# Performance work log

Hardware: AMD Instinct MI355X
Metric: run time of the kernel (lower is better)

## Reference

```python
import jax, jax.numpy as jnp
import numpy as np

SCALE = 8.0  # cfg.TEST_SCALE (eval path)


def setup_inputs() -> dict:
    key = jax.random.key(0)
    ks = jax.random.split(key, 5)
    N, D, F, NC = 65536, 1024, 300, 81
    return {
        "x": jax.random.normal(ks[0], (N, D), dtype=jnp.float32),
        "W_cls": jax.random.normal(ks[1], (1, D), dtype=jnp.float32) * 0.01,
        "b_cls": jnp.zeros((1,), dtype=jnp.float32),
        "W_sem": jax.random.normal(ks[2], (F, D), dtype=jnp.float32) * 0.01,
        "b_sem": jnp.zeros((F,), dtype=jnp.float32),
        "W_bbox": jax.random.normal(ks[3], (NC * 4, D), dtype=jnp.float32) * 0.001,
        "b_bbox": jnp.zeros((NC * 4,), dtype=jnp.float32),
        "sem_matrix": jax.random.normal(ks[4], (NC - 1, F), dtype=jnp.float32),
    }


def reference(x, W_cls, b_cls, W_sem, b_sem, W_bbox, b_bbox, sem_matrix):
    # b_score: Linear(D, 1)
    b_score = x @ W_cls.T + b_cls                      # [N, 1]
    # sem: Linear(D, F)
    sem = x @ W_sem.T + b_sem                          # [N, F]
    # eval path: scale * L2-row-normalized semantic matrix
    sm = SCALE * sem_matrix / jnp.linalg.norm(sem_matrix, axis=1, keepdims=True)
    # the original per-class repeat/mul/sum loop == one GEMM
    cls_score = sem @ sm.T                             # [N, NC-1]
    scores = jnp.concatenate([b_score, cls_score], axis=1)  # [N, NC]
    bbox_deltas = x @ W_bbox.T + b_bbox                # [N, NC*4]
    return (scores, bbox_deltas)
```

## Files before the change

kernel.cpp:

```cpp
#include <hip/hip_runtime.h>
#include <hip/hip_bf16.h>
#include <stdint.h>

#define KDIM 1024
#define NPAD 512
#define NCOLS 405
#define SCORE_COLS 81
#define BBOX_COLS 324
#define NROWS 65536
#define FDIM 300


typedef short v8s __attribute__((ext_vector_type(8)));
typedef float v4f __attribute__((ext_vector_type(4)));

typedef __attribute__((address_space(3))) uint32_t lds_u32_t;
typedef __attribute__((address_space(1))) uint32_t glb_u32_t;

__device__ __forceinline__ void async16(void* lds, const void* g) {
    __builtin_amdgcn_global_load_lds((const glb_u32_t*)g, (lds_u32_t*)lds, 16, 0, 0);
}

__device__ __forceinline__ uint16_t f2bf(float f) {
    union { float f; uint32_t u; } c; c.f = f;
    uint32_t r = c.u + 0x7FFFu + ((c.u >> 16) & 1u);
    return (uint16_t)(r >> 16);
}

__device__ __forceinline__ size_t wt_off(int row, int k) {
    return (size_t)(k >> 5) * (NPAD * 32) + (size_t)row * 32 + (k & 31);
}

__global__ void fill_w(const float* __restrict__ Wcls, const float* __restrict__ bcls,
                       const float* __restrict__ Wbbox, const float* __restrict__ bbbox,
                       uint16_t* __restrict__ Wt, float* __restrict__ bt) {
    int idx = blockIdx.x * 256 + threadIdx.x;
    int row = idx >> 10, k = idx & 1023;
    if (!(row >= 1 && row < 81)) {
        float v;
        if (row == 0) v = Wcls[k];
        else if (row < 81 + BBOX_COLS) v = Wbbox[(size_t)(row - 81) * KDIM + k];
        else v = 0.f;
        Wt[wt_off(row, k)] = f2bf(v);
    }
    if (k == 0 && !(row >= 1 && row < 81)) {
        float b;
        if (row == 0) b = bcls[0];
        else if (row < 81 + BBOX_COLS) b = bbbox[row - 81];
        else b = 0.f;
        bt[row] = b;
    }
}

__global__ void fill_w_sem(const float* __restrict__ Wsem, const float* __restrict__ bsem,
                           const float* __restrict__ semm,
                           uint16_t* __restrict__ Wt, float* __restrict__ bt) {
    const int n = blockIdx.x;
    const int kq = blockIdx.y;
    const int tid = threadIdx.x;
    __shared__ float s_row[FDIM];
    __shared__ float red[256];
    __shared__ float s_scale, s_bdot;

    const float* sr = semm + (size_t)n * FDIM;
    float p = 0.f, pb = 0.f;
    for (int f = tid; f < FDIM; f += 256) {
        float v = sr[f];
        s_row[f] = v;
        p += v * v;
        pb += v * bsem[f];
    }
    red[tid] = p; __syncthreads();
    for (int s = 128; s > 0; s >>= 1) { if (tid < s) red[tid] += red[tid + s]; __syncthreads(); }
    float norm2 = red[0]; __syncthreads();
    red[tid] = pb; __syncthreads();
    for (int s = 128; s > 0; s >>= 1) { if (tid < s) red[tid] += red[tid + s]; __syncthreads(); }
    if (tid == 0) { s_scale = 8.0f / sqrtf(norm2); s_bdot = red[0]; }
    __syncthreads();
    const float scale = s_scale;
    if (kq == 0 && tid == 0) bt[1 + n] = scale * s_bdot;

    const int k = kq * 256 + tid;
    float acc = 0.f;
    #pragma unroll 8
    for (int f = 0; f < FDIM; ++f) acc += s_row[f] * Wsem[(size_t)f * KDIM + k];
    Wt[wt_off(1 + n, k)] = f2bf(scale * acc);
}

#define A_STRIDE 36
#define A_BUF_ELEMS (64 * A_STRIDE)
#define B_BUF_ELEMS (NPAD * 32)
#define SMEM_BYTES (2 * A_BUF_ELEMS * 2 + 2 * B_BUF_ELEMS * 2)

__device__ __forceinline__ void compute_tile(const uint16_t* As, const uint16_t* Bs,
                                             int wc, int l16, int quad,
                                             v4f acc[4][4]) {
    v8s a[4], b[4];
    #pragma unroll
    for (int mi = 0; mi < 4; ++mi)
        a[mi] = *(const v8s*)&As[(mi * 16 + l16) * A_STRIDE + quad * 8];
    #pragma unroll
    for (int ni = 0; ni < 4; ++ni)
        b[ni] = *(const v8s*)&Bs[(wc * 64 + ni * 16 + l16) * 32 + quad * 8];
    #pragma unroll
    for (int mi = 0; mi < 4; ++mi)
        #pragma unroll
        for (int ni = 0; ni < 4; ++ni)
            acc[mi][ni] = __builtin_amdgcn_mfma_f32_16x16x32_bf16(a[mi], b[ni], acc[mi][ni], 0, 0, 0);
}

__global__ __launch_bounds__(512, 4) void gemm_fused(
        const float* __restrict__ x, const uint16_t* __restrict__ Wt,
        const float* __restrict__ bt, float* __restrict__ out) {
    const int tid = threadIdx.x;
    const int wave = tid >> 6, lane = tid & 63;
    const int wc = wave;
    const int quad = lane >> 4, l16 = lane & 15;
    const int mtile = blockIdx.x;

    __shared__ __align__(16) char smem[SMEM_BYTES];
    uint16_t* As = (uint16_t*)smem;
    uint16_t* Bs = (uint16_t*)(smem + 2 * A_BUF_ELEMS * 2);

    const float* xb = x + (size_t)mtile * 64 * KDIM;

    const int colbase = wc * 64;
    float bias[4];
    #pragma unroll
    for (int ni = 0; ni < 4; ++ni) bias[ni] = bt[colbase + ni * 16 + l16];

    v4f acc[4][4];
    #pragma unroll
    for (int mi = 0; mi < 4; ++mi)
        #pragma unroll
        for (int ni = 0; ni < 4; ++ni)
            acc[mi][ni] = v4f{0.f, 0.f, 0.f, 0.f};

    const int am = tid >> 3, akc = tid & 7;
    float4 av;

    #pragma unroll
    for (int i = 0; i < 4; ++i) {
        int c = i * 512 + tid;
        async16(&Bs[0 * B_BUF_ELEMS + c * 8], Wt + (size_t)c * 8);
    }
    av = *(const float4*)(xb + (size_t)am * KDIM + akc * 4);
    {
        __hip_bfloat162 lo = __float22bfloat162_rn(make_float2(av.x, av.y));
        __hip_bfloat162 hi = __float22bfloat162_rn(make_float2(av.z, av.w));
        uint2 p; p.x = *(uint32_t*)&lo; p.y = *(uint32_t*)&hi;
        *(uint2*)&As[0 * A_BUF_ELEMS + am * A_STRIDE + akc * 4] = p;
    }

    for (int kt = 0; kt < 31; ++kt) {
        const int buf = kt & 1;
        __syncthreads();
        #pragma unroll
        for (int i = 0; i < 4; ++i) {
            int c = i * 512 + tid;
            async16(&Bs[(buf ^ 1) * B_BUF_ELEMS + c * 8],
                    Wt + (size_t)(kt + 1) * B_BUF_ELEMS + (size_t)c * 8);
        }
        av = *(const float4*)(xb + (size_t)am * KDIM + (kt + 1) * 32 + akc * 4);
        compute_tile(&As[buf * A_BUF_ELEMS], &Bs[buf * B_BUF_ELEMS], wc, l16, quad, acc);
        {
            __hip_bfloat162 lo = __float22bfloat162_rn(make_float2(av.x, av.y));
            __hip_bfloat162 hi = __float22bfloat162_rn(make_float2(av.z, av.w));
            uint2 p; p.x = *(uint32_t*)&lo; p.y = *(uint32_t*)&hi;
            *(uint2*)&As[(buf ^ 1) * A_BUF_ELEMS + am * A_STRIDE + akc * 4] = p;
        }
    }
    __syncthreads();
    compute_tile(&As[1 * A_BUF_ELEMS], &Bs[1 * B_BUF_ELEMS], wc, l16, quad, acc);

    const int rowbase = mtile * 64;
    float* eps = (float*)smem;
    float* outb = out + (size_t)NROWS * SCORE_COLS;
    #pragma unroll
    for (int h = 0; h < 2; ++h) {
        __syncthreads();
        #pragma unroll
        for (int mi2 = 0; mi2 < 2; ++mi2) {
            const int mi = h * 2 + mi2;
            #pragma unroll
            for (int ni = 0; ni < 4; ++ni) {
                const int col = colbase + ni * 16 + l16;
                if (col < NCOLS) {
                    #pragma unroll
                    for (int r = 0; r < 4; ++r)
                        eps[(mi2 * 16 + quad * 4 + r) * 409 + col] = acc[mi][ni][r] + bias[ni];
                }
            }
        }
        __syncthreads();
        const int row0 = rowbase + h * 32;
        for (int idx = tid; idx < 32 * SCORE_COLS; idx += 512) {
            int r = idx / SCORE_COLS, c = idx - r * SCORE_COLS;
            out[(size_t)(row0 + r) * SCORE_COLS + c] = eps[r * 409 + c];
        }
        for (int idx = tid; idx < 32 * BBOX_COLS; idx += 512) {
            int r = idx / BBOX_COLS, c = idx - r * BBOX_COLS;
            outb[(size_t)(row0 + r) * BBOX_COLS + c] = eps[r * 409 + SCORE_COLS + c];
        }
    }
}

extern "C" void kernel_launch(void* const* d_in, const int* in_sizes, int n_in,
                              void* d_out, int out_size, void* d_ws, size_t ws_size,
                              hipStream_t stream) {
    const float* x     = (const float*)d_in[0];
    const float* Wcls  = (const float*)d_in[1];
    const float* bcls  = (const float*)d_in[2];
    const float* Wsem  = (const float*)d_in[3];
    const float* bsem  = (const float*)d_in[4];
    const float* Wbbox = (const float*)d_in[5];
    const float* bbbox = (const float*)d_in[6];
    const float* semm  = (const float*)d_in[7];
    float* out = (float*)d_out;

    uint16_t* Wt = (uint16_t*)d_ws;
    float*    bt = (float*)((char*)d_ws + (size_t)NPAD * KDIM * 2);

    fill_w<<<dim3(2048), dim3(256), 0, stream>>>(Wcls, bcls, Wbbox, bbbox, Wt, bt);
    fill_w_sem<<<dim3(80, 4), dim3(256), 0, stream>>>(Wsem, bsem, semm, Wt, bt);
    gemm_fused<<<dim3(1024), dim3(512), 0, stream>>>(x, Wt, bt, out);
}
```

Before: 524.7 us.

## Load weight fragments directly from global into registers, skip B LDS staging

The GEMM stops staging the weight tile in LDS. Each wave now loads its bf16 weight fragments straight from global (L2-resident) into registers and prefetches the next k-slab while the MFMAs run. The padded column count drops from 512 to 416, so the last waves skip the MMA work on padding columns. The A tile uses a triple-buffered LDS ring with a single barrier per k-step, and outputs are written with nontemporal stores. Smaller LDS use may allow more resident blocks, but the wave workload is now uneven and every block reads the weights from L2 itself.

```diff
diff --git a/kernel.cpp b/kernel.cpp
--- a/kernel.cpp
+++ b/kernel.cpp
@@ -3,23 +3,17 @@
 #include <stdint.h>
 
 #define KDIM 1024
-#define NPAD 512
+#define NPAD 416
 #define NCOLS 405
 #define SCORE_COLS 81
 #define BBOX_COLS 324
 #define NROWS 65536
 #define FDIM 300
+#define SLAB (NPAD * 32)
 
 
 typedef short v8s __attribute__((ext_vector_type(8)));
 typedef float v4f __attribute__((ext_vector_type(4)));
-
-typedef __attribute__((address_space(3))) uint32_t lds_u32_t;
-typedef __attribute__((address_space(1))) uint32_t glb_u32_t;
-
-__device__ __forceinline__ void async16(void* lds, const void* g) {
-    __builtin_amdgcn_global_load_lds((const glb_u32_t*)g, (lds_u32_t*)lds, 16, 0, 0);
-}
 
 __device__ __forceinline__ uint16_t f2bf(float f) {
     union { float f; uint32_t u; } c; c.f = f;
@@ -28,7 +22,7 @@
 }
 
 __device__ __forceinline__ size_t wt_off(int row, int k) {
-    return (size_t)(k >> 5) * (NPAD * 32) + (size_t)row * 32 + (k & 31);
+    return (size_t)(k >> 5) * SLAB + (size_t)row * 32 + (k & 31);
 }
 
 __global__ void fill_w(const float* __restrict__ Wcls, const float* __restrict__ bcls,
@@ -89,24 +83,14 @@
 
 #define A_STRIDE 36
 #define A_BUF_ELEMS (64 * A_STRIDE)
-#define B_BUF_ELEMS (NPAD * 32)
-#define SMEM_BYTES (2 * A_BUF_ELEMS * 2 + 2 * B_BUF_ELEMS * 2)
-
-__device__ __forceinline__ void compute_tile(const uint16_t* As, const uint16_t* Bs,
-                                             int wc, int l16, int quad,
-                                             v4f acc[4][4]) {
-    v8s a[4], b[4];
-    #pragma unroll
-    for (int mi = 0; mi < 4; ++mi)
-        a[mi] = *(const v8s*)&As[(mi * 16 + l16) * A_STRIDE + quad * 8];
-    #pragma unroll
-    for (int ni = 0; ni < 4; ++ni)
-        b[ni] = *(const v8s*)&Bs[(wc * 64 + ni * 16 + l16) * 32 + quad * 8];
-    #pragma unroll
-    for (int mi = 0; mi < 4; ++mi)
-        #pragma unroll
-        for (int ni = 0; ni < 4; ++ni)
-            acc[mi][ni] = __builtin_amdgcn_mfma_f32_16x16x32_bf16(a[mi], b[ni], acc[mi][ni], 0, 0, 0);
+#define EPS_STRIDE 409
+#define SMEM_BYTES (32 * EPS_STRIDE * 4)
+
+__device__ __forceinline__ void stcvt(uint16_t* p, float4 av) {
+    __hip_bfloat162 lo = __float22bfloat162_rn(make_float2(av.x, av.y));
+    __hip_bfloat162 hi = __float22bfloat162_rn(make_float2(av.z, av.w));
+    uint2 v; v.x = *(uint32_t*)&lo; v.y = *(uint32_t*)&hi;
+    *(uint2*)p = v;
 }
 
 __global__ __launch_bounds__(512, 4) void gemm_fused(
@@ -114,20 +98,15 @@
         const float* __restrict__ bt, float* __restrict__ out) {
     const int tid = threadIdx.x;
     const int wave = tid >> 6, lane = tid & 63;
-    const int wc = wave;
     const int quad = lane >> 4, l16 = lane & 15;
     const int mtile = blockIdx.x;
+    const int NT = (wave < 6) ? 4 : (wave == 6 ? 2 : 0);
 
     __shared__ __align__(16) char smem[SMEM_BYTES];
     uint16_t* As = (uint16_t*)smem;
-    uint16_t* Bs = (uint16_t*)(smem + 2 * A_BUF_ELEMS * 2);
 
     const float* xb = x + (size_t)mtile * 64 * KDIM;
-
-    const int colbase = wc * 64;
-    float bias[4];
-    #pragma unroll
-    for (int ni = 0; ni < 4; ++ni) bias[ni] = bt[colbase + ni * 16 + l16];
+    const int colbase = wave * 64;
 
     v4f acc[4][4];
     #pragma unroll
@@ -137,45 +116,58 @@
             acc[mi][ni] = v4f{0.f, 0.f, 0.f, 0.f};
 
     const int am = tid >> 3, akc = tid & 7;
-    float4 av;
-
-    #pragma unroll
-    for (int i = 0; i < 4; ++i) {
-        int c = i * 512 + tid;
-        async16(&Bs[0 * B_BUF_ELEMS + c * 8], Wt + (size_t)c * 8);
-    }
-    av = *(const float4*)(xb + (size_t)am * KDIM + akc * 4);
-    {
-        __hip_bfloat162 lo = __float22bfloat162_rn(make_float2(av.x, av.y));
-        __hip_bfloat162 hi = __float22bfloat162_rn(make_float2(av.z, av.w));
-        uint2 p; p.x = *(uint32_t*)&lo; p.y = *(uint32_t*)&hi;
-        *(uint2*)&As[0 * A_BUF_ELEMS + am * A_STRIDE + akc * 4] = p;
-    }
-
-    for (int kt = 0; kt < 31; ++kt) {
-        const int buf = kt & 1;
-        __syncthreads();
+    const float* aptr = xb + (size_t)am * KDIM + akc * 4;
+    const uint16_t* bptr = Wt + (size_t)(colbase + l16) * 32 + quad * 8;
+
+    v8s bcur[4];
+
+    float4 av0  = *(const float4*)aptr;
+    float4 av_n = *(const float4*)(aptr + 32);
+    #pragma unroll
+    for (int ni = 0; ni < 4; ++ni)
+        if (ni < NT) bcur[ni] = *(const v8s*)(bptr + ni * 512);
+    stcvt(As + am * A_STRIDE + akc * 4, av0);
+    asm volatile("s_waitcnt lgkmcnt(0)" ::: "memory");
+    __builtin_amdgcn_s_barrier();
+    asm volatile("" ::: "memory");
+
+    int rb = 0, wb = 1;
+    float4 av_nn;
+    for (int kt = 0; kt < 32; ++kt) {
+        if (kt < 30) av_nn = *(const float4*)(aptr + (size_t)(kt + 2) * 32);
+        const uint16_t* Ar = As + rb * A_BUF_ELEMS;
+        v8s a0 = *(const v8s*)(Ar + (0 * 16 + l16) * A_STRIDE + quad * 8);
+        v8s a1 = *(const v8s*)(Ar + (1 * 16 + l16) * A_STRIDE + quad * 8);
+        v8s a2 = *(const v8s*)(Ar + (2 * 16 + l16) * A_STRIDE + quad * 8);
+        v8s a3 = *(const v8s*)(Ar + (3 * 16 + l16) * A_STRIDE + quad * 8);
+        const uint16_t* bnext = bptr + (size_t)(kt + 1) * SLAB;
         #pragma unroll
-        for (int i = 0; i < 4; ++i) {
-            int c = i * 512 + tid;
-            async16(&Bs[(buf ^ 1) * B_BUF_ELEMS + c * 8],
-                    Wt + (size_t)(kt + 1) * B_BUF_ELEMS + (size_t)c * 8);
-        }
-        av = *(const float4*)(xb + (size_t)am * KDIM + (kt + 1) * 32 + akc * 4);
-        compute_tile(&As[buf * A_BUF_ELEMS], &Bs[buf * B_BUF_ELEMS], wc, l16, quad, acc);
-        {
-            __hip_bfloat162 lo = __float22bfloat162_rn(make_float2(av.x, av.y));
-            __hip_bfloat162 hi = __float22bfloat162_rn(make_float2(av.z, av.w));
-            uint2 p; p.x = *(uint32_t*)&lo; p.y = *(uint32_t*)&hi;
-            *(uint2*)&As[(buf ^ 1) * A_BUF_ELEMS + am * A_STRIDE + akc * 4] = p;
-        }
-    }
-    __syncthreads();
-    compute_tile(&As[1 * A_BUF_ELEMS], &Bs[1 * B_BUF_ELEMS], wc, l16, quad, acc);
+        for (int ni = 0; ni < 4; ++ni) {
+            if (ni < NT) {
+                acc[0][ni] = __builtin_amdgcn_mfma_f32_16x16x32_bf16(a0, bcur[ni], acc[0][ni], 0, 0, 0);
+                acc[1][ni] = __builtin_amdgcn_mfma_f32_16x16x32_bf16(a1, bcur[ni], acc[1][ni], 0, 0, 0);
+                acc[2][ni] = __builtin_amdgcn_mfma_f32_16x16x32_bf16(a2, bcur[ni], acc[2][ni], 0, 0, 0);
+                acc[3][ni] = __builtin_amdgcn_mfma_f32_16x16x32_bf16(a3, bcur[ni], acc[3][ni], 0, 0, 0);
+                if (kt < 31) bcur[ni] = *(const v8s*)(bnext + ni * 512);
+            }
+        }
+        if (kt < 31) {
+            stcvt(As + wb * A_BUF_ELEMS + am * A_STRIDE + akc * 4, av_n);
+            av_n = av_nn;
+            asm volatile("s_waitcnt lgkmcnt(0)" ::: "memory");
+            __builtin_amdgcn_s_barrier();
+            asm volatile("" ::: "memory");
+            int ib = 3 - rb - wb; rb = wb; wb = ib;
+        }
+    }
 
     const int rowbase = mtile * 64;
     float* eps = (float*)smem;
     float* outb = out + (size_t)NROWS * SCORE_COLS;
+    float bias[4];
+    #pragma unroll
+    for (int ni = 0; ni < 4; ++ni)
+        bias[ni] = (ni < NT) ? bt[colbase + ni * 16 + l16] : 0.f;
     #pragma unroll
     for (int h = 0; h < 2; ++h) {
         __syncthreads();
@@ -185,10 +177,10 @@
             #pragma unroll
             for (int ni = 0; ni < 4; ++ni) {
                 const int col = colbase + ni * 16 + l16;
-                if (col < NCOLS) {
+                if (ni < NT && col < NCOLS) {
                     #pragma unroll
                     for (int r = 0; r < 4; ++r)
-                        eps[(mi2 * 16 + quad * 4 + r) * 409 + col] = acc[mi][ni][r] + bias[ni];
+                        eps[(mi2 * 16 + quad * 4 + r) * EPS_STRIDE + col] = acc[mi][ni][r] + bias[ni];
                 }
             }
         }
@@ -196,11 +188,13 @@
         const int row0 = rowbase + h * 32;
         for (int idx = tid; idx < 32 * SCORE_COLS; idx += 512) {
             int r = idx / SCORE_COLS, c = idx - r * SCORE_COLS;
-            out[(size_t)(row0 + r) * SCORE_COLS + c] = eps[r * 409 + c];
+            __builtin_nontemporal_store(eps[r * EPS_STRIDE + c],
+                                        &out[(size_t)(row0 + r) * SCORE_COLS + c]);
         }
         for (int idx = tid; idx < 32 * BBOX_COLS; idx += 512) {
             int r = idx / BBOX_COLS, c = idx - r * BBOX_COLS;
-            outb[(size_t)(row0 + r) * BBOX_COLS + c] = eps[r * 409 + SCORE_COLS + c];
+            __builtin_nontemporal_store(eps[r * EPS_STRIDE + SCORE_COLS + c],
+                                        &outb[(size_t)(row0 + r) * BBOX_COLS + c]);
         }
     }
 }
@@ -221,7 +215,7 @@
     uint16_t* Wt = (uint16_t*)d_ws;
     float*    bt = (float*)((char*)d_ws + (size_t)NPAD * KDIM * 2);
 
-    fill_w<<<dim3(2048), dim3(256), 0, stream>>>(Wcls, bcls, Wbbox, bbbox, Wt, bt);
+    fill_w<<<dim3((NPAD * KDIM) / 256), dim3(256), 0, stream>>>(Wcls, bcls, Wbbox, bbbox, Wt, bt);
     fill_w_sem<<<dim3(80, 4), dim3(256), 0, stream>>>(Wsem, bsem, semm, Wt, bt);
-    gemm_fused<<<dim3(1024), dim3(512), 0, stream>>>(x, Wt, bt, out);
-}
+    gemm_fused<<<dim3(NROWS / 64), dim3(512), 0, stream>>>(x, Wt, bt, out);
+}
```

Measured after the change: 493.5 us. -5.9%, faster.
